# Performance work log

Measured on AMD Instinct MI355X. Metric: run time of the kernel, lower is better.

## Reference

```python
import jax, jax.numpy as jnp
import numpy as np

B, S, K, N = 4, 2048, 4096, 4096   # batch, seq, infeatures, outfeatures
GROUP = 128                        # quantization group size along K
N_OUT = 128                        # outlier features (last columns of x)


def setup_inputs() -> dict:
    key = jax.random.key(0)
    ks = jax.random.split(key, 6)
    x = jax.random.normal(ks[0], (B, S, K), dtype=jnp.float32)
    # unpacked 4-bit integer weights in [0, 16)
    qweight = jax.random.randint(ks[1], (N, K), 0, 16, dtype=jnp.int32)
    # per-group scales and scaled zeros: [numgroup, N] = [K//GROUP, N]
    scales = jax.random.uniform(ks[2], (K // GROUP, N), dtype=jnp.float32, minval=0.005, maxval=0.02)
    # scaled_zeros = -zeros * scales in the original pack(); keep them negative-ish
    scaled_zeros = -jax.random.uniform(ks[3], (K // GROUP, N), dtype=jnp.float32, minval=0.0, maxval=0.16)
    oweight = jax.random.normal(ks[4], (N, N_OUT), dtype=jnp.float32) * 0.02
    bias = jax.random.normal(ks[5], (N,), dtype=jnp.float32) * 0.02
    return {"x": x, "qweight": qweight, "scales": scales,
            "scaled_zeros": scaled_zeros, "oweight": oweight, "bias": bias}


def reference(x, qweight, scales, scaled_zeros, oweight, bias):
    # gemm_4bit: dequantize W[n,k] = q[n,k]*scales[k//G, n] + scaled_zeros[k//G, n]
    g = x.shape[-1] // scales.shape[0]
    scales_full = jnp.repeat(scales, g, axis=0).T        # [N, K]
    zeros_full = jnp.repeat(scaled_zeros, g, axis=0).T   # [N, K]
    W = qweight.astype(scales.dtype) * scales_full + zeros_full  # [N, K]
    y = jnp.einsum('bsk,nk->bsn', x, W)
    # fused outlier fp16 linear on the last N_OUT input features + bias
    n_out = oweight.shape[1]
    y = y + jnp.einsum('bso,no->bsn', x[..., -n_out:], oweight) + bias
    return y
```

## Files before the change

### kernel.cpp

```cpp
#include <hip/hip_runtime.h>

#define K_ 4096
#define N_ 4096
#define M_ 8192
#define NOUT_ 128
#define NT_ (K_ / 64)

typedef __bf16 bf16x8 __attribute__((ext_vector_type(8)));
typedef float f32x4 __attribute__((ext_vector_type(4)));
typedef unsigned short ushort8 __attribute__((ext_vector_type(8)));

__device__ __forceinline__ unsigned short f2bf(float f) {
  unsigned u = __builtin_bit_cast(unsigned, f);
  u += 0x7fffu + ((u >> 16) & 1u);
  return (unsigned short)(u >> 16);
}

__global__ void cvt_x_kernel(const float4* __restrict__ x4, ushort8* __restrict__ xb) {
  const int t = blockIdx.x * 256 + threadIdx.x;
  float4 a = x4[2 * t];
  float4 b = x4[2 * t + 1];
  ushort8 o;
  o[0] = f2bf(a.x); o[1] = f2bf(a.y); o[2] = f2bf(a.z); o[3] = f2bf(a.w);
  o[4] = f2bf(b.x); o[5] = f2bf(b.y); o[6] = f2bf(b.z); o[7] = f2bf(b.w);
  xb[t] = o;
}

__global__ void dequant_kernel(const int4* __restrict__ q4,
                               const float* __restrict__ scales,
                               const float* __restrict__ zeros,
                               const float* __restrict__ ow,
                               ushort8* __restrict__ wb) {
  const int t = blockIdx.x * 256 + threadIdx.x;
  const int n = t >> 9;
  const int k = (t & 511) << 3;
  const int g = k >> 7;
  const float s = scales[g * N_ + n];
  const float z = zeros[g * N_ + n];
  int4 qa = q4[2 * t], qb = q4[2 * t + 1];
  float f[8];
  f[0] = qa.x * s + z; f[1] = qa.y * s + z; f[2] = qa.z * s + z; f[3] = qa.w * s + z;
  f[4] = qb.x * s + z; f[5] = qb.y * s + z; f[6] = qb.z * s + z; f[7] = qb.w * s + z;
  if (k >= K_ - NOUT_) {
    const float4* o4 = (const float4*)(ow + n * NOUT_ + (k - (K_ - NOUT_)));
    float4 oa = o4[0], ob = o4[1];
    f[0] += oa.x; f[1] += oa.y; f[2] += oa.z; f[3] += oa.w;
    f[4] += ob.x; f[5] += ob.y; f[6] += ob.z; f[7] += ob.w;
  }
  ushort8 r;
  #pragma unroll
  for (int i = 0; i < 8; ++i) r[i] = f2bf(f[i]);
  wb[t] = r;
}

#define STAGE(dA, dB, kof)                                                          \
  do {                                                                              \
    _Pragma("unroll") for (int i_ = 0; i_ < 4; ++i_)                                \
        __builtin_amdgcn_global_load_lds(                                           \
            (__attribute__((address_space(1))) void*)(gA[i_] + (kof)),              \
            (__attribute__((address_space(3))) void*)((dA) + aoff[i_]), 16, 0, 0);  \
    _Pragma("unroll") for (int i_ = 0; i_ < 4; ++i_)                                \
        __builtin_amdgcn_global_load_lds(                                           \
            (__attribute__((address_space(1))) void*)(gB[i_] + (kof)),              \
            (__attribute__((address_space(3))) void*)((dB) + aoff[i_]), 16, 0, 0);  \
  } while (0)

__global__ __launch_bounds__(512, 2) void gemm_kernel(
    const unsigned short* __restrict__ xb,
    const unsigned short* __restrict__ wb,
    const float* __restrict__ bias,
    float* __restrict__ out) {
  __shared__ __attribute__((aligned(16))) char lds[131072];

  const int tid  = threadIdx.x;
  const int w    = tid >> 6;
  const int lane = tid & 63;
  const int q    = lane >> 4;
  const int l16  = lane & 15;
  const int wr   = w >> 2;
  const int wc   = w & 3;

  const int id  = blockIdx.y * 16 + blockIdx.x;
  const int id2 = (id & 7) * 64 + (id >> 3);
  const int m0  = (id2 >> 4) * 256;
  const int n0  = (id2 & 15) * 256;

  const unsigned short* gA[4];
  const unsigned short* gB[4];
  int aoff[4];
  #pragma unroll
  for (int i = 0; i < 4; ++i) {
    const int o  = i * 8192 + w * 1024 + lane * 16;
    const int r  = o >> 7;
    const int cs = (o >> 4) & 7;
    const int cg = cs ^ (r & 7);
    gA[i] = xb + (size_t)(m0 + r) * K_ + cg * 8;
    gB[i] = wb + (size_t)(n0 + r) * K_ + cg * 8;
    aoff[i] = i * 8192 + w * 1024;
  }

  const char* pA0 = lds + (wr * 128 + l16) * 128;
  const char* pB0 = lds + 65536 + (wc * 64 + l16) * 128;
  const int sl0 = ((0 + q) ^ (l16 & 7)) * 16;
  const int sl1 = ((4 + q) ^ (l16 & 7)) * 16;

  f32x4 acc[8][4] = {};

  STAGE((char*)lds, (char*)lds + 65536, 0);

  for (int t = 0; t < NT_; ++t) {
    const int curo = (t & 1) * 32768;
    const char* cA = pA0 + curo;
    const char* cB = pB0 + curo;

    if (t + 1 < NT_) {
      char* dA = (char*)lds + (((t + 1) & 1) * 32768);
      char* dB = (char*)lds + 65536 + (((t + 1) & 1) * 32768);
      STAGE(dA, dB, (t + 1) * 64);
      asm volatile("s_waitcnt vmcnt(8)" ::: "memory");
    } else {
      asm volatile("s_waitcnt vmcnt(0)" ::: "memory");
    }
    __builtin_amdgcn_s_barrier();
    __builtin_amdgcn_sched_barrier(0);

    bf16x8 a[4][2], b0[2][2], b1[2][2];

    #pragma unroll
    for (int f = 0; f < 4; ++f) {
      a[f][0] = *(const bf16x8*)(cA + f * 2048 + sl0);
      a[f][1] = *(const bf16x8*)(cA + f * 2048 + sl1);
    }
    #pragma unroll
    for (int j = 0; j < 2; ++j) {
      b0[j][0] = *(const bf16x8*)(cB + j * 2048 + sl0);
      b0[j][1] = *(const bf16x8*)(cB + j * 2048 + sl1);
    }
    __builtin_amdgcn_s_barrier();
    __builtin_amdgcn_s_setprio(1);
    #pragma unroll
    for (int f = 0; f < 4; ++f)
      #pragma unroll
      for (int j = 0; j < 2; ++j) {
        acc[f][j] = __builtin_amdgcn_mfma_f32_16x16x32_bf16(a[f][0], b0[j][0], acc[f][j], 0, 0, 0);
        acc[f][j] = __builtin_amdgcn_mfma_f32_16x16x32_bf16(a[f][1], b0[j][1], acc[f][j], 0, 0, 0);
      }
    __builtin_amdgcn_s_setprio(0);
    __builtin_amdgcn_s_barrier();

    #pragma unroll
    for (int j = 0; j < 2; ++j) {
      b1[j][0] = *(const bf16x8*)(cB + (2 + j) * 2048 + sl0);
      b1[j][1] = *(const bf16x8*)(cB + (2 + j) * 2048 + sl1);
    }
    __builtin_amdgcn_s_barrier();
    __builtin_amdgcn_s_setprio(1);
    #pragma unroll
    for (int f = 0; f < 4; ++f)
      #pragma unroll
      for (int j = 0; j < 2; ++j) {
        acc[f][2 + j] = __builtin_amdgcn_mfma_f32_16x16x32_bf16(a[f][0], b1[j][0], acc[f][2 + j], 0, 0, 0);
        acc[f][2 + j] = __builtin_amdgcn_mfma_f32_16x16x32_bf16(a[f][1], b1[j][1], acc[f][2 + j], 0, 0, 0);
      }
    __builtin_amdgcn_s_setprio(0);
    __builtin_amdgcn_s_barrier();

    #pragma unroll
    for (int f = 0; f < 4; ++f) {
      a[f][0] = *(const bf16x8*)(cA + (4 + f) * 2048 + sl0);
      a[f][1] = *(const bf16x8*)(cA + (4 + f) * 2048 + sl1);
    }
    __builtin_amdgcn_s_barrier();
    __builtin_amdgcn_s_setprio(1);
    #pragma unroll
    for (int f = 0; f < 4; ++f)
      #pragma unroll
      for (int j = 0; j < 2; ++j) {
        acc[4 + f][j] = __builtin_amdgcn_mfma_f32_16x16x32_bf16(a[f][0], b0[j][0], acc[4 + f][j], 0, 0, 0);
        acc[4 + f][j] = __builtin_amdgcn_mfma_f32_16x16x32_bf16(a[f][1], b0[j][1], acc[4 + f][j], 0, 0, 0);
      }
    __builtin_amdgcn_s_setprio(0);
    __builtin_amdgcn_s_barrier();

    __builtin_amdgcn_s_setprio(1);
    #pragma unroll
    for (int f = 0; f < 4; ++f)
      #pragma unroll
      for (int j = 0; j < 2; ++j) {
        acc[4 + f][2 + j] = __builtin_amdgcn_mfma_f32_16x16x32_bf16(a[f][0], b1[j][0], acc[4 + f][2 + j], 0, 0, 0);
        acc[4 + f][2 + j] = __builtin_amdgcn_mfma_f32_16x16x32_bf16(a[f][1], b1[j][1], acc[4 + f][2 + j], 0, 0, 0);
      }
    __builtin_amdgcn_s_setprio(0);
    __builtin_amdgcn_s_barrier();
  }

  float bv[4];
  #pragma unroll
  for (int j = 0; j < 4; ++j)
    bv[j] = bias[n0 + wc * 64 + j * 16 + l16];

  #pragma unroll
  for (int i = 0; i < 8; ++i) {
    const int mrow = m0 + wr * 128 + i * 16 + q * 4;
    #pragma unroll
    for (int j = 0; j < 4; ++j) {
      const int n = n0 + wc * 64 + j * 16 + l16;
      float* op = out + (size_t)mrow * N_ + n;
      #pragma unroll
      for (int r = 0; r < 4; ++r)
        op[(size_t)r * N_] = acc[i][j][r] + bv[j];
    }
  }
}

extern "C" void kernel_launch(void* const* d_in, const int* in_sizes, int n_in,
                              void* d_out, int out_size, void* d_ws, size_t ws_size,
                              hipStream_t stream) {
  const float* x      = (const float*)d_in[0];
  const int*   qw     = (const int*)d_in[1];
  const float* scales = (const float*)d_in[2];
  const float* zeros  = (const float*)d_in[3];
  const float* ow     = (const float*)d_in[4];
  const float* bias   = (const float*)d_in[5];
  float* out = (float*)d_out;

  unsigned short* xb = (unsigned short*)d_ws;
  unsigned short* wb = xb + (size_t)M_ * K_;

  cvt_x_kernel<<<(M_ * K_ / 8) / 256, 256, 0, stream>>>((const float4*)x, (ushort8*)xb);
  dequant_kernel<<<(N_ * K_ / 8) / 256, 256, 0, stream>>>((const int4*)qw, scales, zeros, ow,
                                                          (ushort8*)wb);
  dim3 grid(N_ / 256, M_ / 256);
  gemm_kernel<<<grid, 512, 0, stream>>>(xb, wb, bias, out);
}
```

Measured before the change: 552.5 us.

## Split LDS tiles into halves and interleave global-to-LDS loads with MFMA phases

Splits each 256-row A/B tile into two 128-row halves and rearranges the LDS layout so each half can be refilled on its own. The loads for the next and next-next k-steps are issued between MFMA phases instead of all at once at the top of the loop, giving a deeper pipeline across two k-steps. All B fragments for a step are now held in registers at once. The aim is to hide global-memory latency behind compute and remove the stall at the loop head, at the cost of higher register pressure and tricky vmcnt and buffer-reuse ordering.

New measurement: 495.9 us. -10.2%, faster.

```diff
diff --git a/kernel.cpp b/kernel.cpp
--- a/kernel.cpp
+++ b/kernel.cpp
@@ -53,16 +53,27 @@
   wb[t] = r;
 }
 
-#define STAGE(dA, dB, kof)                                                          \
-  do {                                                                              \
-    _Pragma("unroll") for (int i_ = 0; i_ < 4; ++i_)                                \
-        __builtin_amdgcn_global_load_lds(                                           \
-            (__attribute__((address_space(1))) void*)(gA[i_] + (kof)),              \
-            (__attribute__((address_space(3))) void*)((dA) + aoff[i_]), 16, 0, 0);  \
-    _Pragma("unroll") for (int i_ = 0; i_ < 4; ++i_)                                \
-        __builtin_amdgcn_global_load_lds(                                           \
-            (__attribute__((address_space(1))) void*)(gB[i_] + (kof)),              \
-            (__attribute__((address_space(3))) void*)((dB) + aoff[i_]), 16, 0, 0);  \
+#define AS1 __attribute__((address_space(1)))
+#define AS3 __attribute__((address_space(3)))
+
+#define STAGE_A(h, kt, ubase)                                                      \
+  do {                                                                             \
+    __builtin_amdgcn_global_load_lds(                                              \
+        (AS1 void*)(sgA0 + (size_t)(h) * 128 * K_ + (kt) * 64),                    \
+        (AS3 void*)((ubase) + w * 1024), 16, 0, 0);                                \
+    __builtin_amdgcn_global_load_lds(                                              \
+        (AS1 void*)(sgA1 + (size_t)(h) * 128 * K_ + (kt) * 64),                    \
+        (AS3 void*)((ubase) + 8192 + w * 1024), 16, 0, 0);                         \
+  } while (0)
+
+#define STAGE_B(h, kt, ubase)                                                      \
+  do {                                                                             \
+    __builtin_amdgcn_global_load_lds(                                              \
+        (AS1 void*)(sgB0 + (size_t)(h) * 128 * K_ + (kt) * 64),                    \
+        (AS3 void*)((ubase) + w * 1024), 16, 0, 0);                                \
+    __builtin_amdgcn_global_load_lds(                                              \
+        (AS1 void*)(sgB1 + (size_t)(h) * 128 * K_ + (kt) * 64),                    \
+        (AS3 void*)((ubase) + 8192 + w * 1024), 16, 0, 0);                         \
   } while (0)
 
 __global__ __launch_bounds__(512, 2) void gemm_kernel(
@@ -70,7 +81,7 @@
     const unsigned short* __restrict__ wb,
     const float* __restrict__ bias,
     float* __restrict__ out) {
-  __shared__ __attribute__((aligned(16))) char lds[131072];
+  __shared__ __attribute__((aligned(16))) char smem[131072];
 
   const int tid  = threadIdx.x;
   const int w    = tid >> 6;
@@ -85,46 +96,38 @@
   const int m0  = (id2 >> 4) * 256;
   const int n0  = (id2 & 15) * 256;
 
-  const unsigned short* gA[4];
-  const unsigned short* gB[4];
-  int aoff[4];
-  #pragma unroll
-  for (int i = 0; i < 4; ++i) {
-    const int o  = i * 8192 + w * 1024 + lane * 16;
-    const int r  = o >> 7;
-    const int cs = (o >> 4) & 7;
-    const int cg = cs ^ (r & 7);
-    gA[i] = xb + (size_t)(m0 + r) * K_ + cg * 8;
-    gB[i] = wb + (size_t)(n0 + r) * K_ + cg * 8;
-    aoff[i] = i * 8192 + w * 1024;
-  }
-
-  const char* pA0 = lds + (wr * 128 + l16) * 128;
-  const char* pB0 = lds + 65536 + (wc * 64 + l16) * 128;
+  const int rr = w * 8 + (lane >> 3);
+  const int cg = (lane & 7) ^ ((lane >> 3) & 7);
+  const unsigned short* sgA0 = xb + (size_t)(m0 + rr) * K_ + cg * 8;
+  const unsigned short* sgA1 = xb + (size_t)(m0 + 64 + rr) * K_ + cg * 8;
+  const unsigned short* sgB0 = wb + (size_t)(n0 + rr) * K_ + cg * 8;
+  const unsigned short* sgB1 = wb + (size_t)(n0 + 64 + rr) * K_ + cg * 8;
+
+  const char* pA_base = smem + wr * 16384 + l16 * 128;
+  const char* pB_base = smem + 65536 + (wc >> 1) * 16384 +
+                        ((wc & 1) * 64 + l16) * 128;
   const int sl0 = ((0 + q) ^ (l16 & 7)) * 16;
   const int sl1 = ((4 + q) ^ (l16 & 7)) * 16;
 
   f32x4 acc[8][4] = {};
 
-  STAGE((char*)lds, (char*)lds + 65536, 0);
+  STAGE_B(0, 0, smem + 65536);
+  STAGE_B(1, 0, smem + 65536 + 16384);
+  STAGE_A(0, 0, smem);
+  STAGE_A(1, 0, smem + 16384);
+  STAGE_B(0, 1, smem + 65536 + 32768);
+  STAGE_B(1, 1, smem + 65536 + 32768 + 16384);
+  STAGE_A(0, 1, smem + 32768);
+  asm volatile("s_waitcnt vmcnt(6)" ::: "memory");
+  __builtin_amdgcn_s_barrier();
 
   for (int t = 0; t < NT_; ++t) {
     const int curo = (t & 1) * 32768;
-    const char* cA = pA0 + curo;
-    const char* cB = pB0 + curo;
-
-    if (t + 1 < NT_) {
-      char* dA = (char*)lds + (((t + 1) & 1) * 32768);
-      char* dB = (char*)lds + 65536 + (((t + 1) & 1) * 32768);
-      STAGE(dA, dB, (t + 1) * 64);
-      asm volatile("s_waitcnt vmcnt(8)" ::: "memory");
-    } else {
-      asm volatile("s_waitcnt vmcnt(0)" ::: "memory");
-    }
-    __builtin_amdgcn_s_barrier();
-    __builtin_amdgcn_sched_barrier(0);
-
-    bf16x8 a[4][2], b0[2][2], b1[2][2];
+    const int nxto = ((t + 1) & 1) * 32768;
+    const char* cA = pA_base + curo;
+    const char* cB = pB_base + curo;
+
+    bf16x8 a[4][2], b[4][2];
 
     #pragma unroll
     for (int f = 0; f < 4; ++f) {
@@ -132,65 +135,72 @@
       a[f][1] = *(const bf16x8*)(cA + f * 2048 + sl1);
     }
     #pragma unroll
-    for (int j = 0; j < 2; ++j) {
-      b0[j][0] = *(const bf16x8*)(cB + j * 2048 + sl0);
-      b0[j][1] = *(const bf16x8*)(cB + j * 2048 + sl1);
-    }
-    __builtin_amdgcn_s_barrier();
-    __builtin_amdgcn_s_setprio(1);
-    #pragma unroll
-    for (int f = 0; f < 4; ++f)
-      #pragma unroll
-      for (int j = 0; j < 2; ++j) {
-        acc[f][j] = __builtin_amdgcn_mfma_f32_16x16x32_bf16(a[f][0], b0[j][0], acc[f][j], 0, 0, 0);
-        acc[f][j] = __builtin_amdgcn_mfma_f32_16x16x32_bf16(a[f][1], b0[j][1], acc[f][j], 0, 0, 0);
-      }
-    __builtin_amdgcn_s_setprio(0);
-    __builtin_amdgcn_s_barrier();
-
-    #pragma unroll
-    for (int j = 0; j < 2; ++j) {
-      b1[j][0] = *(const bf16x8*)(cB + (2 + j) * 2048 + sl0);
-      b1[j][1] = *(const bf16x8*)(cB + (2 + j) * 2048 + sl1);
-    }
-    __builtin_amdgcn_s_barrier();
-    __builtin_amdgcn_s_setprio(1);
-    #pragma unroll
-    for (int f = 0; f < 4; ++f)
-      #pragma unroll
-      for (int j = 0; j < 2; ++j) {
-        acc[f][2 + j] = __builtin_amdgcn_mfma_f32_16x16x32_bf16(a[f][0], b1[j][0], acc[f][2 + j], 0, 0, 0);
-        acc[f][2 + j] = __builtin_amdgcn_mfma_f32_16x16x32_bf16(a[f][1], b1[j][1], acc[f][2 + j], 0, 0, 0);
+    for (int j = 0; j < 4; ++j) {
+      b[j][0] = *(const bf16x8*)(cB + j * 2048 + sl0);
+      b[j][1] = *(const bf16x8*)(cB + j * 2048 + sl1);
+    }
+    if (t + 1 < NT_) STAGE_A(1, t + 1, smem + nxto + 16384);
+    __builtin_amdgcn_s_barrier();
+    asm volatile("s_waitcnt lgkmcnt(0)" ::: "memory");
+    __builtin_amdgcn_sched_barrier(0);
+    __builtin_amdgcn_s_setprio(1);
+    #pragma unroll
+    for (int f = 0; f < 4; ++f)
+      #pragma unroll
+      for (int j = 0; j < 2; ++j) {
+        acc[f][j] = __builtin_amdgcn_mfma_f32_16x16x32_bf16(a[f][0], b[j][0], acc[f][j], 0, 0, 0);
+        acc[f][j] = __builtin_amdgcn_mfma_f32_16x16x32_bf16(a[f][1], b[j][1], acc[f][j], 0, 0, 0);
+      }
+    __builtin_amdgcn_s_setprio(0);
+    __builtin_amdgcn_s_barrier();
+
+    if (t + 2 < NT_) STAGE_B(0, t + 2, smem + 65536 + curo);
+    __builtin_amdgcn_s_setprio(1);
+    #pragma unroll
+    for (int f = 0; f < 4; ++f)
+      #pragma unroll
+      for (int j = 0; j < 2; ++j) {
+        acc[f][2 + j] = __builtin_amdgcn_mfma_f32_16x16x32_bf16(a[f][0], b[2 + j][0], acc[f][2 + j], 0, 0, 0);
+        acc[f][2 + j] = __builtin_amdgcn_mfma_f32_16x16x32_bf16(a[f][1], b[2 + j][1], acc[f][2 + j], 0, 0, 0);
       }
     __builtin_amdgcn_s_setprio(0);
     __builtin_amdgcn_s_barrier();
 
     #pragma unroll
     for (int f = 0; f < 4; ++f) {
-      a[f][0] = *(const bf16x8*)(cA + (4 + f) * 2048 + sl0);
-      a[f][1] = *(const bf16x8*)(cA + (4 + f) * 2048 + sl1);
-    }
-    __builtin_amdgcn_s_barrier();
-    __builtin_amdgcn_s_setprio(1);
-    #pragma unroll
-    for (int f = 0; f < 4; ++f)
-      #pragma unroll
-      for (int j = 0; j < 2; ++j) {
-        acc[4 + f][j] = __builtin_amdgcn_mfma_f32_16x16x32_bf16(a[f][0], b0[j][0], acc[4 + f][j], 0, 0, 0);
-        acc[4 + f][j] = __builtin_amdgcn_mfma_f32_16x16x32_bf16(a[f][1], b0[j][1], acc[4 + f][j], 0, 0, 0);
-      }
-    __builtin_amdgcn_s_setprio(0);
-    __builtin_amdgcn_s_barrier();
-
-    __builtin_amdgcn_s_setprio(1);
-    #pragma unroll
-    for (int f = 0; f < 4; ++f)
-      #pragma unroll
-      for (int j = 0; j < 2; ++j) {
-        acc[4 + f][2 + j] = __builtin_amdgcn_mfma_f32_16x16x32_bf16(a[f][0], b1[j][0], acc[4 + f][2 + j], 0, 0, 0);
-        acc[4 + f][2 + j] = __builtin_amdgcn_mfma_f32_16x16x32_bf16(a[f][1], b1[j][1], acc[4 + f][2 + j], 0, 0, 0);
-      }
-    __builtin_amdgcn_s_setprio(0);
+      a[f][0] = *(const bf16x8*)(cA + 8192 + f * 2048 + sl0);
+      a[f][1] = *(const bf16x8*)(cA + 8192 + f * 2048 + sl1);
+    }
+    if (t + 2 < NT_) STAGE_B(1, t + 2, smem + 65536 + curo + 16384);
+    __builtin_amdgcn_s_barrier();
+    asm volatile("s_waitcnt lgkmcnt(0)" ::: "memory");
+    __builtin_amdgcn_sched_barrier(0);
+    __builtin_amdgcn_s_setprio(1);
+    #pragma unroll
+    for (int f = 0; f < 4; ++f)
+      #pragma unroll
+      for (int j = 0; j < 2; ++j) {
+        acc[4 + f][j] = __builtin_amdgcn_mfma_f32_16x16x32_bf16(a[f][0], b[j][0], acc[4 + f][j], 0, 0, 0);
+        acc[4 + f][j] = __builtin_amdgcn_mfma_f32_16x16x32_bf16(a[f][1], b[j][1], acc[4 + f][j], 0, 0, 0);
+      }
+    __builtin_amdgcn_s_setprio(0);
+    __builtin_amdgcn_s_barrier();
+
+    if (t + 2 < NT_) STAGE_A(0, t + 2, smem + curo);
+    __builtin_amdgcn_s_setprio(1);
+    #pragma unroll
+    for (int f = 0; f < 4; ++f)
+      #pragma unroll
+      for (int j = 0; j < 2; ++j) {
+        acc[4 + f][2 + j] = __builtin_amdgcn_mfma_f32_16x16x32_bf16(a[f][0], b[2 + j][0], acc[4 + f][2 + j], 0, 0, 0);
+        acc[4 + f][2 + j] = __builtin_amdgcn_mfma_f32_16x16x32_bf16(a[f][1], b[2 + j][1], acc[4 + f][2 + j], 0, 0, 0);
+      }
+    __builtin_amdgcn_s_setprio(0);
+    if (t + 2 < NT_) {
+      asm volatile("s_waitcnt vmcnt(6)" ::: "memory");
+    } else {
+      asm volatile("s_waitcnt vmcnt(0)" ::: "memory");
+    }
     __builtin_amdgcn_s_barrier();
   }
 
```
